# Performance work log

Hardware: AMD Instinct MI355X
Metric: run time of the kernel (lower is better)

## Reference

```python
import jax, jax.numpy as jnp
import numpy as np

# Dimensions
T = 1024      # tokens
D = 1024      # d_model
DFF = 1024    # expert intermediate dim
R = 64        # tucker rank (r_in == r_out)
G = 8         # n_group
E = 32        # experts_per_group
NEXP = G * E  # 256 routed experts
K = 8         # top-k


def setup_inputs() -> dict:
    key = jax.random.key(0)
    ks = jax.random.split(key, 12)
    s = 0.02
    return {
        "x": jax.random.normal(ks[0], (T, D), jnp.float32),
        "Wg": jax.random.normal(ks[1], (D, NEXP), jnp.float32) * s,
        "uin_gate": jax.random.normal(ks[2], (G, D, R), jnp.float32) * s,
        "core_gate": jax.random.normal(ks[3], (G, E, R, R), jnp.float32) * s,
        "uout_gate": jax.random.normal(ks[4], (G, R, DFF), jnp.float32) * s,
        "uin_up": jax.random.normal(ks[5], (G, D, R), jnp.float32) * s,
        "core_up": jax.random.normal(ks[6], (G, E, R, R), jnp.float32) * s,
        "uout_up": jax.random.normal(ks[7], (G, R, DFF), jnp.float32) * s,
        "uin_down": jax.random.normal(ks[8], (G, DFF, R), jnp.float32) * s,
        "core_down": jax.random.normal(ks[9], (G, E, R, R), jnp.float32) * s,
        "uout_down": jax.random.normal(ks[10], (G, R, D), jnp.float32) * s,
    }


def _moe_forward(x, Wg, uin_gate, core_gate, uout_gate,
                 uin_up, core_up, uout_up,
                 uin_down, core_down, uout_down):
    Tn, d = x.shape
    # Router: top-k over 256 experts, softmax over the k logits (fp32 as in torch)
    logits = x @ Wg                                   # [T, NEXP]
    w, sel = jax.lax.top_k(logits, K)                 # [T, K]
    w = jax.nn.softmax(w.astype(jnp.float32), axis=-1).astype(x.dtype)

    e = sel.reshape(-1)                               # [F] global expert id
    g = e // E                                        # [F] group id
    tok = jnp.repeat(jnp.arange(Tn), K)               # [F] source token id
    mask = (g[:, None] == jnp.arange(G)[None, :]).astype(x.dtype)  # [F, G]

    def gather_in(uin):
        # project tokens with every group's u_in once, then gather per pair
        pre = jnp.einsum('td,gdr->gtr', x, uin)       # [G, T, R]
        return pre[g, tok]                            # [F, R]

    def core_apply(xin, core):
        # per-pair Tucker core slice bmm: x.unsqueeze(1) @ core[rel_idx]
        slices = core.reshape(G * E, R, R)[e]         # [F, R, R] gather
        return jnp.einsum('fr,fro->fo', xin, slices)  # [F, R]

    def group_out(h, U):
        # per-pair group-specific projection: h[f] @ U[g_f]
        out = jnp.zeros((h.shape[0], U.shape[-1]), h.dtype)
        for gi in range(G):  # fixed small loop over 8 groups
            out = out + (h * mask[:, gi:gi + 1]) @ U[gi]
        return out

    gate_h = group_out(core_apply(gather_in(uin_gate), core_gate), uout_gate)  # [F, DFF]
    up_h = group_out(core_apply(gather_in(uin_up), core_up), uout_up)          # [F, DFF]
    act = jax.nn.silu(gate_h) * up_h                                           # SwiGLU
    xin_d = group_out(act, uin_down)                                           # [F, R]
    out_f = group_out(core_apply(xin_d, core_down), uout_down)                 # [F, D]
    out_f = out_f * w.reshape(-1)[:, None]
    # scatter-add expert outputs back to tokens
    return jax.ops.segment_sum(out_f, tok, num_segments=Tn)


def reference(x, Wg, uin_gate, core_gate, uout_gate,
              uin_up, core_up, uout_up,
              uin_down, core_down, uout_down):
    return _moe_forward(x, Wg, uin_gate, core_gate, uout_gate,
                        uin_up, core_up, uout_up,
                        uin_down, core_down, uout_down)
```

## Files before the change

### kernel.cpp

```cpp
#include <hip/hip_runtime.h>
#include <hip/hip_bf16.h>
#include <math.h>


#define T_ 1024
#define D_ 1024
#define DFF_ 1024
#define R_ 64
#define G_ 8
#define E_ 32
#define NEXP_ 256
#define K_ 8
#define F_ 8192
#define LKZ_ 8
#define LTB_ 8
#define PKZ_ 2
#define DKZ_ 4
#define LP_ 72

typedef short bf16x8 __attribute__((ext_vector_type(8)));
typedef float f32x4 __attribute__((ext_vector_type(4)));

__device__ __forceinline__ unsigned short f2bf(float f) {
  unsigned int u = __float_as_uint(f);
  u += 0x7fffu + ((u >> 16) & 1u);
  return (unsigned short)(u >> 16);
}

__device__ __forceinline__ void stage_tile(short* dst, const unsigned short* src,
                                           int gp, int tid) {
  for (int idx = tid; idx < 512; idx += 256) {
    int r = idx >> 3, c8 = (idx & 7) << 3;
    *(uint4*)&dst[r * LP_ + c8] = *(const uint4*)&src[(size_t)r * gp + c8];
  }
}

__device__ __forceinline__ void stage_tile_guard(short* dst, const unsigned short* src,
                                                 int gp, int rows_valid, int tid) {
  for (int idx = tid; idx < 512; idx += 256) {
    int r = idx >> 3, c8 = (idx & 7) << 3;
    uint4 v = make_uint4(0u, 0u, 0u, 0u);
    if (r < rows_valid) v = *(const uint4*)&src[(size_t)r * gp + c8];
    *(uint4*)&dst[r * LP_ + c8] = v;
  }
}

__device__ __forceinline__ void mma_strip(const short* As, const short* Bs,
                                          int ms, int lane, f32x4* acc) {
  int lm = lane & 15;
  int lk = (lane >> 4) << 3;
#pragma unroll
  for (int kc = 0; kc < 64; kc += 32) {
    bf16x8 a = *(const bf16x8*)&As[(ms + lm) * LP_ + kc + lk];
#pragma unroll
    for (int nt = 0; nt < 4; ++nt) {
      bf16x8 b = *(const bf16x8*)&Bs[(nt * 16 + lm) * LP_ + kc + lk];
      acc[nt] = __builtin_amdgcn_mfma_f32_16x16x32_bf16(a, b, acc[nt], 0, 0, 0);
    }
  }
}

__global__ __launch_bounds__(256) void k_prep_logits(
    const float* __restrict__ x, const float* __restrict__ Wg,
    const float* __restrict__ s0, const float* __restrict__ s1,
    const float* __restrict__ s2, const float* __restrict__ s3,
    const float* __restrict__ s4, const float* __restrict__ s5,
    unsigned short* __restrict__ xb,
    unsigned short* __restrict__ d0, unsigned short* __restrict__ d1,
    unsigned short* __restrict__ d2, unsigned short* __restrict__ d3,
    unsigned short* __restrict__ d4, unsigned short* __restrict__ d5,
    int* __restrict__ cnt, float* __restrict__ lp) {
  __shared__ float shbuf[64 * 65];
  int b = blockIdx.x;
  if (b < 896) {
    int id = b >> 7, rem = b & 127, g = rem >> 4, tile = rem & 15;
    if (id == 6) {
      size_t base = ((size_t)g * 16 + tile) * 8192;
      for (int i = threadIdx.x; i < 2048; i += 256) {
        size_t idx = base + (size_t)i * 4;
        float4 v = *(const float4*)&x[idx];
        xb[idx + 0] = f2bf(v.x);
        xb[idx + 1] = f2bf(v.y);
        xb[idx + 2] = f2bf(v.z);
        xb[idx + 3] = f2bf(v.w);
      }
      if (g == 0 && tile == 0) cnt[threadIdx.x] = 0;
      return;
    }
    const float* src = id == 0 ? s0 : id == 1 ? s1 : id == 2 ? s2 : id == 3 ? s3 : id == 4 ? s4 : s5;
    unsigned short* dst = id == 0 ? d0 : id == 1 ? d1 : id == 2 ? d2 : id == 3 ? d3 : id == 4 ? d4 : d5;
    if (id < 3) {
      int r0 = tile * 64;
      for (int idx = threadIdx.x; idx < 4096; idx += 256) {
        int r = idx >> 6, c = idx & 63;
        shbuf[r * 65 + c] = src[((size_t)g * 1024 + r0 + r) * 64 + c];
      }
      __syncthreads();
      for (int idx = threadIdx.x; idx < 4096; idx += 256) {
        int c = idx >> 6, r = idx & 63;
        dst[((size_t)g * 64 + c) * 1024 + r0 + r] = f2bf(shbuf[r * 65 + c]);
      }
    } else {
      int c0 = tile * 64;
      for (int idx = threadIdx.x; idx < 4096; idx += 256) {
        int r = idx >> 6, c = idx & 63;
        shbuf[r * 65 + c] = src[((size_t)g * 64 + r) * 1024 + c0 + c];
      }
      __syncthreads();
      for (int idx = threadIdx.x; idx < 4096; idx += 256) {
        int c = idx >> 6, r = idx & 63;
        dst[((size_t)g * 1024 + c0 + c) * 64 + r] = f2bf(shbuf[r * 65 + c]);
      }
    }
    return;
  }
  int lb = b - 896;
  int t0 = (lb & 127) * LTB_;
  int z = lb >> 7;
  int e = threadIdx.x;
  float* xs = shbuf;
  float a[LTB_] = {};
  int dc = z * 128;
  {
    int idx = threadIdx.x * 4;
    int tl = idx >> 7, d = idx & 127;
    *(float4*)&xs[tl * 128 + d] = *(const float4*)&x[(size_t)(t0 + tl) * D_ + dc + d];
  }
  __syncthreads();
#pragma unroll 8
  for (int d2 = 0; d2 < 128; ++d2) {
    float wv = Wg[(size_t)(dc + d2) * NEXP_ + e];
#pragma unroll
    for (int j = 0; j < LTB_; ++j) a[j] = fmaf(xs[j * 128 + d2], wv, a[j]);
  }
  size_t base = (size_t)z * T_ * NEXP_;
#pragma unroll
  for (int j = 0; j < LTB_; ++j)
    lp[base + (size_t)(t0 + j) * NEXP_ + e] = a[j];
}

__global__ __launch_bounds__(256) void k_pre_topk(
    const unsigned short* __restrict__ xb,
    const unsigned short* __restrict__ uinT_g, const unsigned short* __restrict__ uinT_u,
    const float* __restrict__ lp,
    float* __restrict__ Pgp, float* __restrict__ Pup,
    int* __restrict__ sel, float* __restrict__ wsm, int* __restrict__ cnt) {
  __shared__ short sh2[2 * 64 * LP_];
  int b = blockIdx.x;
  if (b < 512) {
    int tile = b & 15, g = (b >> 4) & 7, zz = b >> 7;
    int gu = zz >> 1, kz = zz & 1;
    const unsigned short* U = gu ? uinT_u : uinT_g;
    float* P = gu ? Pup : Pgp;
    int t0 = tile * 64;
    short* As = sh2;
    short* Bs = sh2 + 64 * LP_;
    int tid = threadIdx.x, lane = tid & 63, ms = (tid >> 6) * 16;
    f32x4 acc[4] = {};
    int dlo = kz * (D_ / PKZ_);
    for (int dc = dlo; dc < dlo + D_ / PKZ_; dc += 64) {
      stage_tile(As, xb + (size_t)t0 * D_ + dc, D_, tid);
      stage_tile(Bs, U + (size_t)g * 64 * 1024 + dc, 1024, tid);
      __syncthreads();
      mma_strip(As, Bs, ms, lane, acc);
      __syncthreads();
    }
    int lm = lane & 15, lq = (lane >> 4) * 4;
#pragma unroll
    for (int nt = 0; nt < 4; ++nt)
#pragma unroll
      for (int r = 0; r < 4; ++r)
        P[((size_t)(kz * G_ + g) * T_ + t0 + ms + lq + r) * R_ + nt * 16 + lm] = acc[nt][r];
    return;
  }
  int tb = b - 512;
  int wave = threadIdx.x >> 6;
  int lane = threadIdx.x & 63;
  int t = tb * 4 + wave;
  float v[4];
  int idx[4];
#pragma unroll
  for (int j = 0; j < 4; ++j) {
    idx[j] = lane + 64 * j;
    float s = 0.f;
#pragma unroll
    for (int z = 0; z < LKZ_; ++z)
      s += lp[(size_t)z * T_ * NEXP_ + (size_t)t * NEXP_ + idx[j]];
    v[j] = s;
  }
  float topv[K_];
  int topi[K_];
#pragma unroll
  for (int k = 0; k < K_; ++k) {
    float bv = v[0];
    int bi = idx[0];
#pragma unroll
    for (int j = 1; j < 4; ++j)
      if (v[j] > bv || (v[j] == bv && idx[j] < bi)) { bv = v[j]; bi = idx[j]; }
#pragma unroll
    for (int off = 32; off > 0; off >>= 1) {
      float ov = __shfl_xor(bv, off);
      int oi = __shfl_xor(bi, off);
      if (ov > bv || (ov == bv && oi < bi)) { bv = ov; bi = oi; }
    }
    topv[k] = bv;
    topi[k] = bi;
#pragma unroll
    for (int j = 0; j < 4; ++j)
      if (idx[j] == bi) v[j] = -INFINITY;
  }
  float m = topv[0];
  float ev[K_];
  float s = 0.f;
#pragma unroll
  for (int k = 0; k < K_; ++k) { ev[k] = expf(topv[k] - m); s += ev[k]; }
  float inv = 1.f / s;
  if (lane < K_) {
    sel[t * K_ + lane] = topi[lane];
    wsm[t * K_ + lane] = ev[lane] * inv;
    atomicAdd(&cnt[topi[lane]], 1);
  }
}

__global__ __launch_bounds__(1024) void k_sortscan(const int* __restrict__ cnt,
                                                   const int* __restrict__ sel,
                                                   const float* __restrict__ wsm,
                                                   int* __restrict__ off,
                                                   int* __restrict__ stok,
                                                   int* __restrict__ se,
                                                   float* __restrict__ sw,
                                                   int* __restrict__ ipos) {
  __shared__ int s[NEXP_];
  __shared__ int offl[NEXP_];
  __shared__ int curl[NEXP_];
  int i = threadIdx.x;
  if (i < NEXP_) s[i] = cnt[i];
  __syncthreads();
  for (int d = 1; d < NEXP_; d <<= 1) {
    int v = 0;
    if (i < NEXP_ && i >= d) v = s[i - d];
    __syncthreads();
    if (i < NEXP_) s[i] += v;
    __syncthreads();
  }
  if (i < NEXP_) {
    offl[i] = s[i] - cnt[i];
    curl[i] = 0;
    off[i + 1] = s[i];
    if (i == 0) off[0] = 0;
  }
  __syncthreads();
  for (int f = i; f < F_; f += 1024) {
    int e = sel[f];
    int p = offl[e] + atomicAdd(&curl[e], 1);
    stok[p] = f >> 3;
    se[p] = e;
    sw[p] = wsm[f];
    ipos[f] = p;
  }
}

__global__ __launch_bounds__(256) void k_core_gu(const float* __restrict__ Pgp,
                                                 const float* __restrict__ Pup,
                                                 const float* __restrict__ core_g,
                                                 const float* __restrict__ core_u,
                                                 const int* __restrict__ stok,
                                                 const int* __restrict__ se,
                                                 unsigned short* __restrict__ xgb,
                                                 unsigned short* __restrict__ xub) {
  int pl = threadIdx.x >> 6;
  int o = threadIdx.x & 63;
  int p = blockIdx.x * 4 + pl;
  int e = se[p];
  int t = stok[p];
  int g = e >> 5;
  __shared__ float rg[4][64], ru[4][64];
  float sg = 0.f, su = 0.f;
#pragma unroll
  for (int kz = 0; kz < PKZ_; ++kz) {
    sg += Pgp[((size_t)(kz * G_ + g) * T_ + t) * R_ + o];
    su += Pup[((size_t)(kz * G_ + g) * T_ + t) * R_ + o];
  }
  rg[pl][o] = sg;
  ru[pl][o] = su;
  __syncthreads();
  const float* cg = core_g + (size_t)e * R_ * R_;
  const float* cu = core_u + (size_t)e * R_ * R_;
  float ag = 0.f, au = 0.f;
#pragma unroll 8
  for (int r = 0; r < R_; ++r) {
    ag = fmaf(rg[pl][r], cg[r * R_ + o], ag);
    au = fmaf(ru[pl][r], cu[r * R_ + o], au);
  }
  xgb[(size_t)p * R_ + o] = f2bf(ag);
  xub[(size_t)p * R_ + o] = f2bf(au);
}

__global__ __launch_bounds__(256) void k_fused_ad(const unsigned short* __restrict__ xgb,
                                                  const unsigned short* __restrict__ xub,
                                                  const unsigned short* __restrict__ uoutT_g,
                                                  const unsigned short* __restrict__ uoutT_u,
                                                  const unsigned short* __restrict__ uinT_d,
                                                  const int* __restrict__ off,
                                                  float* __restrict__ xdp) {
  int g = blockIdx.y;
  int kz = blockIdx.z;
  int p0 = off[g * E_];
  int pend = off[g * E_ + E_];
  int ntiles = (pend - p0 + 63) >> 6;
  __shared__ short Ag[64 * LP_], Au[64 * LP_];
  __shared__ short Bg[64 * LP_], Bu[64 * LP_], Bd[64 * LP_];
  __shared__ short Pt[64 * LP_];
  int tid = threadIdx.x, lane = tid & 63, ms = (tid >> 6) * 16;
  int lm = lane & 15, lq = (lane >> 4) * 4;
  for (int tile = blockIdx.x; tile < ntiles; tile += gridDim.x) {
    int pbase = p0 + tile * 64;
    int rv = pend - pbase; if (rv > 64) rv = 64;
    stage_tile_guard(Ag, xgb + (size_t)pbase * R_, R_, rv, tid);
    stage_tile_guard(Au, xub + (size_t)pbase * R_, R_, rv, tid);
    f32x4 accd[4] = {};
#pragma unroll
    for (int c4 = 0; c4 < 4; ++c4) {
      int cc = kz * (DFF_ / DKZ_) + c4 * 64;
      stage_tile(Bg, uoutT_g + ((size_t)g * DFF_ + cc) * R_, R_, tid);
      stage_tile(Bu, uoutT_u + ((size_t)g * DFF_ + cc) * R_, R_, tid);
      stage_tile(Bd, uinT_d + (size_t)g * 64 * 1024 + cc, 1024, tid);
      __syncthreads();
      f32x4 accg[4] = {}, accu[4] = {};
      mma_strip(Ag, Bg, ms, lane, accg);
      mma_strip(Au, Bu, ms, lane, accu);
#pragma unroll
      for (int nt = 0; nt < 4; ++nt)
#pragma unroll
        for (int r = 0; r < 4; ++r) {
          float gv = accg[nt][r];
          float av = gv / (1.f + expf(-gv)) * accu[nt][r];
          Pt[(ms + lq + r) * LP_ + nt * 16 + lm] = (short)f2bf(av);
        }
      mma_strip(Pt, Bd, ms, lane, accd);
      __syncthreads();
    }
#pragma unroll
    for (int nt = 0; nt < 4; ++nt)
#pragma unroll
      for (int r = 0; r < 4; ++r) {
        int p = pbase + ms + lq + r;
        if (p < pend) xdp[((size_t)kz * F_ + p) * R_ + nt * 16 + lm] = accd[nt][r];
      }
    __syncthreads();
  }
}

__global__ __launch_bounds__(256) void k_core_down(const float* __restrict__ xdp,
                                                   const float* __restrict__ core_d,
                                                   const int* __restrict__ se,
                                                   unsigned short* __restrict__ xd2b) {
  int pl = threadIdx.x >> 6;
  int o = threadIdx.x & 63;
  int p = blockIdx.x * 4 + pl;
  int e = se[p];
  __shared__ float rg[4][64];
  float s = 0.f;
#pragma unroll
  for (int kz = 0; kz < DKZ_; ++kz) s += xdp[((size_t)kz * F_ + p) * R_ + o];
  rg[pl][o] = s;
  __syncthreads();
  const float* cd = core_d + (size_t)e * R_ * R_;
  float a = 0.f;
#pragma unroll 8
  for (int r = 0; r < R_; ++r) a = fmaf(rg[pl][r], cd[r * R_ + o], a);
  xd2b[(size_t)p * R_ + o] = f2bf(a);
}

__global__ __launch_bounds__(256) void k_outf_mfma(const unsigned short* __restrict__ xd2b,
                                                   const unsigned short* __restrict__ uoutT_d,
                                                   const int* __restrict__ off,
                                                   const float* __restrict__ sw,
                                                   float* __restrict__ outf) {
  int g = blockIdx.y;
  int p0 = off[g * E_];
  int pend = off[g * E_ + E_];
  int ntiles = (pend - p0 + 63) >> 6;
  int c0 = blockIdx.z * 64;
  __shared__ short As[64 * LP_], Bs[64 * LP_];
  __shared__ float Os[64 * 68];
  int tid = threadIdx.x, lane = tid & 63, ms = (tid >> 6) * 16;
  int lm = lane & 15, lq = (lane >> 4) * 4;
  for (int tile = blockIdx.x; tile < ntiles; tile += gridDim.x) {
    int pbase = p0 + tile * 64;
    int rv = pend - pbase; if (rv > 64) rv = 64;
    stage_tile_guard(As, xd2b + (size_t)pbase * R_, R_, rv, tid);
    stage_tile(Bs, uoutT_d + ((size_t)g * D_ + c0) * R_, R_, tid);
    __syncthreads();
    f32x4 acc[4] = {};
    mma_strip(As, Bs, ms, lane, acc);
    float wv[4];
#pragma unroll
    for (int r = 0; r < 4; ++r) {
      int p = pbase + ms + lq + r;
      wv[r] = (p < pend) ? sw[p] : 0.f;
    }
#pragma unroll
    for (int nt = 0; nt < 4; ++nt)
#pragma unroll
      for (int r = 0; r < 4; ++r)
        Os[(ms + lq + r) * 68 + nt * 16 + lm] = acc[nt][r] * wv[r];
    __syncthreads();
    for (int idx = tid; idx < 1024; idx += 256) {
      int r = idx >> 4, c4 = (idx & 15) << 2;
      if (r < rv)
        *(float4*)&outf[(size_t)(pbase + r) * D_ + c0 + c4] = *(const float4*)&Os[r * 68 + c4];
    }
    __syncthreads();
  }
}

__global__ __launch_bounds__(256) void k_gather(const float* __restrict__ outf,
                                                const int* __restrict__ ipos,
                                                float* __restrict__ out) {
  int t = blockIdx.x;
  __shared__ int pos[K_];
  if (threadIdx.x < K_) pos[threadIdx.x] = ipos[t * K_ + threadIdx.x];
  __syncthreads();
  int c = threadIdx.x * 4;
  float4 s = make_float4(0.f, 0.f, 0.f, 0.f);
#pragma unroll
  for (int k = 0; k < K_; ++k) {
    float4 v = *(const float4*)(outf + (size_t)pos[k] * D_ + c);
    s.x += v.x; s.y += v.y; s.z += v.z; s.w += v.w;
  }
  *(float4*)(out + (size_t)t * D_ + c) = s;
}

extern "C" void kernel_launch(void* const* d_in, const int* in_sizes, int n_in,
                              void* d_out, int out_size, void* d_ws, size_t ws_size,
                              hipStream_t stream) {
  const float* x = (const float*)d_in[0];
  const float* Wg = (const float*)d_in[1];
  const float* uin_gate = (const float*)d_in[2];
  const float* core_gate = (const float*)d_in[3];
  const float* uout_gate = (const float*)d_in[4];
  const float* uin_up = (const float*)d_in[5];
  const float* core_up = (const float*)d_in[6];
  const float* uout_up = (const float*)d_in[7];
  const float* uin_down = (const float*)d_in[8];
  const float* core_down = (const float*)d_in[9];
  const float* uout_down = (const float*)d_in[10];
  float* out = (float*)d_out;

  char* ws = (char*)d_ws;
  size_t o = 0;
  auto alloc = [&](size_t bytes) { size_t r = o; o = (o + bytes + 255) & ~(size_t)255; return r; };
  size_t o_lp = alloc((size_t)LKZ_ * T_ * NEXP_ * 4);
  size_t o_sel = alloc(F_ * 4);
  size_t o_wsm = alloc(F_ * 4);
  size_t o_cnt = alloc(NEXP_ * 4);
  size_t o_off = alloc((NEXP_ + 1) * 4);
  size_t o_stok = alloc(F_ * 4);
  size_t o_se = alloc(F_ * 4);
  size_t o_sw = alloc(F_ * 4);
  size_t o_ipos = alloc(F_ * 4);
  size_t o_xb = alloc((size_t)T_ * D_ * 2);
  size_t o_uinT_g = alloc((size_t)G_ * 64 * 1024 * 2);
  size_t o_uinT_u = alloc((size_t)G_ * 64 * 1024 * 2);
  size_t o_uinT_d = alloc((size_t)G_ * 64 * 1024 * 2);
  size_t o_uoutT_g = alloc((size_t)G_ * 1024 * 64 * 2);
  size_t o_uoutT_u = alloc((size_t)G_ * 1024 * 64 * 2);
  size_t o_uoutT_d = alloc((size_t)G_ * 1024 * 64 * 2);
  size_t o_xgb = alloc((size_t)F_ * R_ * 2);
  size_t o_xub = alloc((size_t)F_ * R_ * 2);
  size_t o_xd2b = alloc((size_t)F_ * R_ * 2);
  size_t o_pgp = alloc((size_t)PKZ_ * G_ * T_ * R_ * 4);
  size_t o_pup = alloc((size_t)PKZ_ * G_ * T_ * R_ * 4);
  size_t o_xdp = alloc((size_t)DKZ_ * F_ * R_ * 4);
  size_t o_outf = alloc((size_t)F_ * D_ * 4);
  (void)ws_size;

  float* lp = (float*)(ws + o_lp);
  int* sel = (int*)(ws + o_sel);
  float* wsm = (float*)(ws + o_wsm);
  int* cnt = (int*)(ws + o_cnt);
  int* off = (int*)(ws + o_off);
  int* stok = (int*)(ws + o_stok);
  int* se = (int*)(ws + o_se);
  float* sw = (float*)(ws + o_sw);
  int* ipos = (int*)(ws + o_ipos);
  unsigned short* xb = (unsigned short*)(ws + o_xb);
  unsigned short* uinT_g = (unsigned short*)(ws + o_uinT_g);
  unsigned short* uinT_u = (unsigned short*)(ws + o_uinT_u);
  unsigned short* uinT_d = (unsigned short*)(ws + o_uinT_d);
  unsigned short* uoutT_g = (unsigned short*)(ws + o_uoutT_g);
  unsigned short* uoutT_u = (unsigned short*)(ws + o_uoutT_u);
  unsigned short* uoutT_d = (unsigned short*)(ws + o_uoutT_d);
  unsigned short* xgb = (unsigned short*)(ws + o_xgb);
  unsigned short* xub = (unsigned short*)(ws + o_xub);
  unsigned short* xd2b = (unsigned short*)(ws + o_xd2b);
  float* pgp = (float*)(ws + o_pgp);
  float* pup = (float*)(ws + o_pup);
  float* xdp = (float*)(ws + o_xdp);
  float* outf = (float*)(ws + o_outf);

  k_prep_logits<<<1920, 256, 0, stream>>>(x, Wg, uin_gate, uin_up, uin_down,
                                          uout_gate, uout_up, uout_down, xb,
                                          uinT_g, uinT_u, uinT_d,
                                          uoutT_g, uoutT_u, uoutT_d, cnt, lp);
  k_pre_topk<<<768, 256, 0, stream>>>(xb, uinT_g, uinT_u, lp, pgp, pup, sel, wsm, cnt);
  k_sortscan<<<1, 1024, 0, stream>>>(cnt, sel, wsm, off, stok, se, sw, ipos);
  k_core_gu<<<F_ / 4, 256, 0, stream>>>(pgp, pup, core_gate, core_up, stok, se, xgb, xub);
  k_fused_ad<<<dim3(16, G_, DKZ_), 256, 0, stream>>>(xgb, xub, uoutT_g, uoutT_u, uinT_d, off, xdp);
  k_core_down<<<F_ / 4, 256, 0, stream>>>(xdp, core_down, se, xd2b);
  k_outf_mfma<<<dim3(16, G_, D_ / 64), 256, 0, stream>>>(xd2b, uoutT_d, off, sw, outf);
  k_gather<<<T_, 256, 0, stream>>>(outf, ipos, out);
}
```

Baseline: 225.6 us.

## Reduce rank-space outputs per token before the final down projection

The down projection is reassociated: each token's routed rank-64 vectors are weighted and summed per group into a T×512 buffer, then a single dense GEMM against the concatenated group uout_down matrices produces the output. This drops the F×D fp32 intermediate and the separate gather kernel, cutting about 32MB of writes and reads and eightfold redundant projection work. In exchange the per-group sum is rounded to bf16 before the GEMM, which changes numerics slightly.

```diff
diff --git a/kernel.cpp b/kernel.cpp
--- a/kernel.cpp
+++ b/kernel.cpp
@@ -25,6 +25,9 @@
   unsigned int u = __float_as_uint(f);
   u += 0x7fffu + ((u >> 16) & 1u);
   return (unsigned short)(u >> 16);
+}
+__device__ __forceinline__ float bf2f(unsigned short h) {
+  return __uint_as_float((unsigned int)h << 16);
 }
 
 __device__ __forceinline__ void stage_tile(short* dst, const unsigned short* src,
@@ -107,9 +110,16 @@
         shbuf[r * 65 + c] = src[((size_t)g * 64 + r) * 1024 + c0 + c];
       }
       __syncthreads();
-      for (int idx = threadIdx.x; idx < 4096; idx += 256) {
-        int c = idx >> 6, r = idx & 63;
-        dst[((size_t)g * 1024 + c0 + c) * 64 + r] = f2bf(shbuf[r * 65 + c]);
+      if (id == 5) {
+        for (int idx = threadIdx.x; idx < 4096; idx += 256) {
+          int c = idx >> 6, r = idx & 63;
+          dst[(size_t)(c0 + c) * 512 + g * 64 + r] = f2bf(shbuf[r * 65 + c]);
+        }
+      } else {
+        for (int idx = threadIdx.x; idx < 4096; idx += 256) {
+          int c = idx >> 6, r = idx & 63;
+          dst[((size_t)g * 1024 + c0 + c) * 64 + r] = f2bf(shbuf[r * 65 + c]);
+        }
       }
     }
     return;
@@ -372,64 +382,52 @@
   xd2b[(size_t)p * R_ + o] = f2bf(a);
 }
 
-__global__ __launch_bounds__(256) void k_outf_mfma(const unsigned short* __restrict__ xd2b,
-                                                   const unsigned short* __restrict__ uoutT_d,
-                                                   const int* __restrict__ off,
-                                                   const float* __restrict__ sw,
-                                                   float* __restrict__ outf) {
-  int g = blockIdx.y;
-  int p0 = off[g * E_];
-  int pend = off[g * E_ + E_];
-  int ntiles = (pend - p0 + 63) >> 6;
-  int c0 = blockIdx.z * 64;
+__global__ __launch_bounds__(256) void k_accY(const unsigned short* __restrict__ xd2b,
+                                              const int* __restrict__ ipos,
+                                              const int* __restrict__ se,
+                                              const float* __restrict__ sw,
+                                              unsigned short* __restrict__ Ybf) {
+  int t = blockIdx.x * 4 + (threadIdx.x >> 6);
+  int o = threadIdx.x & 63;
+  float y[G_] = {};
+#pragma unroll
+  for (int k = 0; k < K_; ++k) {
+    int p = ipos[t * K_ + k];
+    int g = se[p] >> 5;
+    y[g] += sw[p] * bf2f(xd2b[(size_t)p * R_ + o]);
+  }
+#pragma unroll
+  for (int g = 0; g < G_; ++g)
+    Ybf[(size_t)t * 512 + g * 64 + o] = f2bf(y[g]);
+}
+
+__global__ __launch_bounds__(256) void k_fin(const unsigned short* __restrict__ Ybf,
+                                             const unsigned short* __restrict__ Uod2T,
+                                             float* __restrict__ out) {
+  int t0 = blockIdx.x * 64;
+  int d0 = blockIdx.y * 64;
   __shared__ short As[64 * LP_], Bs[64 * LP_];
   __shared__ float Os[64 * 68];
   int tid = threadIdx.x, lane = tid & 63, ms = (tid >> 6) * 16;
   int lm = lane & 15, lq = (lane >> 4) * 4;
-  for (int tile = blockIdx.x; tile < ntiles; tile += gridDim.x) {
-    int pbase = p0 + tile * 64;
-    int rv = pend - pbase; if (rv > 64) rv = 64;
-    stage_tile_guard(As, xd2b + (size_t)pbase * R_, R_, rv, tid);
-    stage_tile(Bs, uoutT_d + ((size_t)g * D_ + c0) * R_, R_, tid);
+  f32x4 acc[4] = {};
+  for (int kc = 0; kc < 512; kc += 64) {
+    stage_tile(As, Ybf + (size_t)t0 * 512 + kc, 512, tid);
+    stage_tile(Bs, Uod2T + (size_t)d0 * 512 + kc, 512, tid);
     __syncthreads();
-    f32x4 acc[4] = {};
     mma_strip(As, Bs, ms, lane, acc);
-    float wv[4];
-#pragma unroll
-    for (int r = 0; r < 4; ++r) {
-      int p = pbase + ms + lq + r;
-      wv[r] = (p < pend) ? sw[p] : 0.f;
-    }
-#pragma unroll
-    for (int nt = 0; nt < 4; ++nt)
-#pragma unroll
-      for (int r = 0; r < 4; ++r)
-        Os[(ms + lq + r) * 68 + nt * 16 + lm] = acc[nt][r] * wv[r];
     __syncthreads();
-    for (int idx = tid; idx < 1024; idx += 256) {
-      int r = idx >> 4, c4 = (idx & 15) << 2;
-      if (r < rv)
-        *(float4*)&outf[(size_t)(pbase + r) * D_ + c0 + c4] = *(const float4*)&Os[r * 68 + c4];
-    }
-    __syncthreads();
-  }
-}
-
-__global__ __launch_bounds__(256) void k_gather(const float* __restrict__ outf,
-                                                const int* __restrict__ ipos,
-                                                float* __restrict__ out) {
-  int t = blockIdx.x;
-  __shared__ int pos[K_];
-  if (threadIdx.x < K_) pos[threadIdx.x] = ipos[t * K_ + threadIdx.x];
+  }
+#pragma unroll
+  for (int nt = 0; nt < 4; ++nt)
+#pragma unroll
+    for (int r = 0; r < 4; ++r)
+      Os[(ms + lq + r) * 68 + nt * 16 + lm] = acc[nt][r];
   __syncthreads();
-  int c = threadIdx.x * 4;
-  float4 s = make_float4(0.f, 0.f, 0.f, 0.f);
-#pragma unroll
-  for (int k = 0; k < K_; ++k) {
-    float4 v = *(const float4*)(outf + (size_t)pos[k] * D_ + c);
-    s.x += v.x; s.y += v.y; s.z += v.z; s.w += v.w;
-  }
-  *(float4*)(out + (size_t)t * D_ + c) = s;
+  for (int idx = tid; idx < 1024; idx += 256) {
+    int r = idx >> 4, c4 = (idx & 15) << 2;
+    *(float4*)&out[(size_t)(t0 + r) * D_ + d0 + c4] = *(const float4*)&Os[r * 68 + c4];
+  }
 }
 
 extern "C" void kernel_launch(void* const* d_in, const int* in_sizes, int n_in,
@@ -466,14 +464,14 @@
   size_t o_uinT_d = alloc((size_t)G_ * 64 * 1024 * 2);
   size_t o_uoutT_g = alloc((size_t)G_ * 1024 * 64 * 2);
   size_t o_uoutT_u = alloc((size_t)G_ * 1024 * 64 * 2);
-  size_t o_uoutT_d = alloc((size_t)G_ * 1024 * 64 * 2);
+  size_t o_Uod2T = alloc((size_t)D_ * 512 * 2);
   size_t o_xgb = alloc((size_t)F_ * R_ * 2);
   size_t o_xub = alloc((size_t)F_ * R_ * 2);
   size_t o_xd2b = alloc((size_t)F_ * R_ * 2);
+  size_t o_Y = alloc((size_t)T_ * 512 * 2);
   size_t o_pgp = alloc((size_t)PKZ_ * G_ * T_ * R_ * 4);
   size_t o_pup = alloc((size_t)PKZ_ * G_ * T_ * R_ * 4);
   size_t o_xdp = alloc((size_t)DKZ_ * F_ * R_ * 4);
-  size_t o_outf = alloc((size_t)F_ * D_ * 4);
   (void)ws_size;
 
   float* lp = (float*)(ws + o_lp);
@@ -491,24 +489,24 @@
   unsigned short* uinT_d = (unsigned short*)(ws + o_uinT_d);
   unsigned short* uoutT_g = (unsigned short*)(ws + o_uoutT_g);
   unsigned short* uoutT_u = (unsigned short*)(ws + o_uoutT_u);
-  unsigned short* uoutT_d = (unsigned short*)(ws + o_uoutT_d);
+  unsigned short* Uod2T = (unsigned short*)(ws + o_Uod2T);
   unsigned short* xgb = (unsigned short*)(ws + o_xgb);
   unsigned short* xub = (unsigned short*)(ws + o_xub);
   unsigned short* xd2b = (unsigned short*)(ws + o_xd2b);
+  unsigned short* Ybf = (unsigned short*)(ws + o_Y);
   float* pgp = (float*)(ws + o_pgp);
   float* pup = (float*)(ws + o_pup);
   float* xdp = (float*)(ws + o_xdp);
-  float* outf = (float*)(ws + o_outf);
 
   k_prep_logits<<<1920, 256, 0, stream>>>(x, Wg, uin_gate, uin_up, uin_down,
                                           uout_gate, uout_up, uout_down, xb,
                                           uinT_g, uinT_u, uinT_d,
-                                          uoutT_g, uoutT_u, uoutT_d, cnt, lp);
+                                          uoutT_g, uoutT_u, Uod2T, cnt, lp);
   k_pre_topk<<<768, 256, 0, stream>>>(xb, uinT_g, uinT_u, lp, pgp, pup, sel, wsm, cnt);
   k_sortscan<<<1, 1024, 0, stream>>>(cnt, sel, wsm, off, stok, se, sw, ipos);
   k_core_gu<<<F_ / 4, 256, 0, stream>>>(pgp, pup, core_gate, core_up, stok, se, xgb, xub);
   k_fused_ad<<<dim3(16, G_, DKZ_), 256, 0, stream>>>(xgb, xub, uoutT_g, uoutT_u, uinT_d, off, xdp);
   k_core_down<<<F_ / 4, 256, 0, stream>>>(xdp, core_down, se, xd2b);
-  k_outf_mfma<<<dim3(16, G_, D_ / 64), 256, 0, stream>>>(xd2b, uoutT_d, off, sw, outf);
-  k_gather<<<T_, 256, 0, stream>>>(outf, ipos, out);
-}
+  k_accY<<<T_ / 4, 256, 0, stream>>>(xd2b, ipos, se, sw, Ybf);
+  k_fin<<<dim3(16, 16), 256, 0, stream>>>(Ybf, Uod2T, out);
+}
```

Result: faster. 221.2 us (-2.0%).
